# Performance work log

Hardware: AMD Instinct MI355X
Metric: run time of the kernel (lower is better)

Reference implementation:

```python
import jax, jax.numpy as jnp
import numpy as np

B, F, T, EPT, S, E, H, LVL = 16384, 512, 4, 2, 2, 256, 128, 2

def _ple_level(xs_task, x_sh, w_task, b_task, w_sh, b_sh, w_gate, b_gate, w_gsh=None, b_gsh=None):
    # xs_task: [T,B,I] per-task inputs; x_sh: [B,I] shared input
    task_out = jax.nn.relu(jnp.einsum('tbi,teio->tbeo', xs_task, w_task) + b_task[:, None])  # [T,B,EPT,E]
    sh_out = jax.nn.relu(jnp.einsum('bi,sio->bso', x_sh, w_sh) + b_sh)                       # [B,S,E]
    t = task_out.shape[0]
    experts = jnp.concatenate([task_out, jnp.broadcast_to(sh_out[None], (t,) + sh_out.shape)], axis=2)  # [T,B,EPT+S,E]
    gate = jax.nn.softmax(jnp.einsum('tbi,tig->tbg', xs_task, w_gate) + b_gate[:, None], axis=-1)
    task_next = jnp.einsum('tbg,tbge->tbe', gate, experts)  # [T,B,E]
    sh_next = None
    if w_gsh is not None:
        # all experts ordered task0_exp0, task0_exp1, task1_exp0, ..., then shared
        bsz = x_sh.shape[0]
        all_exp = jnp.concatenate([jnp.transpose(task_out, (1, 0, 2, 3)).reshape(bsz, -1, task_out.shape[-1]), sh_out], axis=1)
        gsh = jax.nn.softmax(x_sh @ w_gsh + b_gsh, axis=-1)
        sh_next = jnp.einsum('bg,bge->be', gsh, all_exp)
    return task_next, sh_next

def setup_inputs() -> dict:
    key = jax.random.key(0)
    ks = jax.random.split(key, 16)
    sc = 0.02
    d = {
        'x': jax.random.normal(ks[0], (B, F), jnp.float32),
        # level 0 (in_dim=F, has shared gate)
        'w_task0': jax.random.normal(ks[1], (T, EPT, F, E), jnp.float32) * sc,
        'b_task0': jnp.zeros((T, EPT, E), jnp.float32),
        'w_sh0': jax.random.normal(ks[2], (S, F, E), jnp.float32) * sc,
        'b_sh0': jnp.zeros((S, E), jnp.float32),
        'w_gate0': jax.random.normal(ks[3], (T, F, EPT + S), jnp.float32) * sc,
        'b_gate0': jnp.zeros((T, EPT + S), jnp.float32),
        'w_gsh0': jax.random.normal(ks[4], (F, T * EPT + S), jnp.float32) * sc,
        'b_gsh0': jnp.zeros((T * EPT + S,), jnp.float32),
        # level 1 (last; in_dim=E, no shared gate)
        'w_task1': jax.random.normal(ks[5], (T, EPT, E, E), jnp.float32) * sc,
        'b_task1': jnp.zeros((T, EPT, E), jnp.float32),
        'w_sh1': jax.random.normal(ks[6], (S, E, E), jnp.float32) * sc,
        'b_sh1': jnp.zeros((S, E), jnp.float32),
        'w_gate1': jax.random.normal(ks[7], (T, E, EPT + S), jnp.float32) * sc,
        'b_gate1': jnp.zeros((T, EPT + S), jnp.float32),
        # towers
        'w_tw': jax.random.normal(ks[8], (T, E, H), jnp.float32) * sc,
        'b_tw': jnp.zeros((T, H), jnp.float32),
        'w_out': jax.random.normal(ks[9], (T, H, 2), jnp.float32) * sc,
        'b_out': jnp.zeros((T, 2), jnp.float32),
    }
    return d

def reference(x, w_task0, b_task0, w_sh0, b_sh0, w_gate0, b_gate0, w_gsh0, b_gsh0,
              w_task1, b_task1, w_sh1, b_sh1, w_gate1, b_gate1,
              w_tw, b_tw, w_out, b_out):
    xs_task = jnp.broadcast_to(x[None], (T,) + x.shape)  # all tasks see same input at level 0
    t1, sh1 = _ple_level(xs_task, x, w_task0, b_task0, w_sh0, b_sh0, w_gate0, b_gate0, w_gsh0, b_gsh0)
    t2, _ = _ple_level(t1, sh1, w_task1, b_task1, w_sh1, b_sh1, w_gate1, b_gate1)
    h = jax.nn.relu(jnp.einsum('tbe,teh->tbh', t2, w_tw) + b_tw[:, None])
    logits = jnp.einsum('tbh,tho->tbo', h, w_out) + b_out[:, None]
    p = jax.nn.softmax(logits, axis=-1)
    return jnp.clip(p, 1e-15, 1.0 - 1e-15)  # [T,B,2]
```

## Files before the change

### kernel.cpp

```cpp
#include <hip/hip_runtime.h>

typedef unsigned short u16;
typedef __bf16 bf16x8 __attribute__((ext_vector_type(8)));
typedef float f32x4 __attribute__((ext_vector_type(4)));
typedef u16 u16x8 __attribute__((ext_vector_type(8)));

#define B_ 16384

__device__ __forceinline__ u16 f2b(float f){
  unsigned u = __builtin_bit_cast(unsigned, f);
  u = (u + 0x7FFFu + ((u >> 16) & 1u)) >> 16;
  return (u16)u;
}
__device__ __forceinline__ float b2f(u16 v){
  return __builtin_bit_cast(float, ((unsigned)v) << 16);
}
__device__ __forceinline__ void ld8(const u16* __restrict__ p, float* f){
  u16x8 v = *(const u16x8*)p;
  #pragma unroll
  for (int j = 0; j < 8; ++j) f[j] = b2f(v[j]);
}
__device__ __forceinline__ void st8(u16* __restrict__ p, const float* f){
  u16x8 v;
  #pragma unroll
  for (int j = 0; j < 8; ++j) v[j] = f2b(f[j]);
  *(u16x8*)p = v;
}

__device__ __forceinline__ void gload16(const u16* g, u16* lds){
  __builtin_amdgcn_global_load_lds(
      (const __attribute__((address_space(1))) unsigned int*)g,
      (__attribute__((address_space(3))) unsigned int*)lds, 16, 0, 0);
}

__device__ __forceinline__ void core32(const u16* __restrict__ A,
                                       const u16* __restrict__ Wt,
                                       int K, int m0, int n0, int nt,
                                       u16* sm, f32x4 acc[4][4])
{
  const int tid = threadIdx.x, lane = tid & 63, wave = tid >> 6;
  const int wm = ((tid >> 7) & 3) * 64;
  const int wn = ((tid >> 6) & 1) * 64;

  #pragma unroll
  for (int m = 0; m < 4; ++m)
    #pragma unroll
    for (int n = 0; n < 4; ++n) acc[m][n] = (f32x4){0.f, 0.f, 0.f, 0.f};

  const int s_    = (lane & 7) ^ ((lane >> 3) & 7);
  const int srow2 = 2 * (lane >> 3) + (s_ >> 2);
  const int sk    = (s_ & 3) * 8;
  const u16* gsrc[3];
  int gdst[3];
  #pragma unroll
  for (int i = 0; i < 3; ++i) {
    int c = wave * 3 + i;
    if (c < 16) {
      gsrc[i] = A + (size_t)(m0 + c * 16 + srow2) * K + sk;
      gdst[i] = c * 512;
    } else {
      gsrc[i] = Wt + (size_t)(n0 + (c - 16) * 16 + srow2) * K + sk;
      gdst[i] = 8192 + (c - 16) * 512;
    }
  }

  int aoff[4], boff[4];
  #pragma unroll
  for (int m = 0; m < 4; ++m) {
    int r = wm + m * 16 + (lane & 15);
    int L = r >> 1;
    int phys = (((r & 1) << 2) + (lane >> 4)) ^ (L & 7);
    aoff[m] = L * 64 + phys * 8;
  }
  #pragma unroll
  for (int n = 0; n < 4; ++n) {
    int r = wn + n * 16 + (lane & 15);
    int L = r >> 1;
    int phys = (((r & 1) << 2) + (lane >> 4)) ^ (L & 7);
    boff[n] = 8192 + L * 64 + phys * 8;
  }

  #pragma unroll
  for (int j = 0; j < 2; ++j) {
    u16* sl = sm + j * 12288;
    #pragma unroll
    for (int i = 0; i < 3; ++i) gload16(gsrc[i] + j * 32, sl + gdst[i]);
  }
  asm volatile("s_waitcnt vmcnt(3)" ::: "memory");
  __builtin_amdgcn_s_barrier();

  int cs = 0;
  for (int j = 0; j < nt; ++j) {
    if (j + 2 < nt) {
      int ns = cs + 2; ns = (ns >= 3) ? ns - 3 : ns;
      u16* sl = sm + ns * 12288;
      #pragma unroll
      for (int i = 0; i < 3; ++i) gload16(gsrc[i] + (size_t)(j + 2) * 32, sl + gdst[i]);
    }
    const u16* sa = sm + cs * 12288;
    bf16x8 av[4], bv[4];
    #pragma unroll
    for (int m = 0; m < 4; ++m) av[m] = *(const bf16x8*)(sa + aoff[m]);
    #pragma unroll
    for (int n = 0; n < 4; ++n) bv[n] = *(const bf16x8*)(sa + boff[n]);
    __builtin_amdgcn_s_setprio(1);
    #pragma unroll
    for (int m = 0; m < 4; ++m)
      #pragma unroll
      for (int n = 0; n < 4; ++n)
        acc[m][n] = __builtin_amdgcn_mfma_f32_16x16x32_bf16(av[m], bv[n], acc[m][n], 0, 0, 0);
    __builtin_amdgcn_s_setprio(0);
    if (j + 2 < nt)      asm volatile("s_waitcnt vmcnt(3)" ::: "memory");
    else if (j + 1 < nt) asm volatile("s_waitcnt vmcnt(0)" ::: "memory");
    __builtin_amdgcn_s_barrier();
    cs = (cs == 2) ? 0 : cs + 1;
  }
}


__global__ __launch_bounds__(512) void k_gemm0(const u16* __restrict__ xb,
    const u16* __restrict__ Wt0, const float* __restrict__ bias0,
    u16* __restrict__ E0, float* __restrict__ G0L)
{
  __shared__ __align__(16) u16 sm[36864];
  f32x4 acc[4][4];
  const int bid = blockIdx.x;
  const int swz = (bid & 7) * 168 + (bid >> 3);
  const int m0 = (swz / 21) * 256, n0 = (swz % 21) * 128;
  core32(xb, Wt0, 512, m0, n0, 16, sm, acc);
  const int lane = threadIdx.x & 63;
  const int wm = ((threadIdx.x >> 7) & 3) * 64, wn = ((threadIdx.x >> 6) & 1) * 64;
  #pragma unroll
  for (int mi = 0; mi < 4; ++mi)
    #pragma unroll
    for (int ni = 0; ni < 4; ++ni) {
      int gcol = n0 + wn + ni * 16 + (lane & 15);
      float bias = bias0[gcol];
      #pragma unroll
      for (int q = 0; q < 4; ++q) {
        int grow = m0 + wm + mi * 16 + ((lane >> 4) << 2) + q;
        float v = acc[mi][ni][q] + bias;
        if (gcol < 2560)      E0[(size_t)grow * 2560 + gcol] = f2b(fmaxf(v, 0.f));
        else if (gcol < 2586) G0L[(size_t)grow * 26 + (gcol - 2560)] = v;
      }
    }
}

__global__ __launch_bounds__(256) void k_mix0(const u16* __restrict__ E0,
    const float* __restrict__ G0L, const float* __restrict__ WG1T,
    const float* __restrict__ b_gate1, u16* __restrict__ T1SH,
    float* __restrict__ G1S)
{
  const int b = blockIdx.x * 8 + (threadIdx.x >> 5);
  const int e0 = (threadIdx.x & 31) * 8;
  const float* gl = G0L + (size_t)b * 26;
  float g[4][4];
  #pragma unroll
  for (int t = 0; t < 4; ++t) {
    float l0 = gl[t*4+0], l1 = gl[t*4+1], l2 = gl[t*4+2], l3 = gl[t*4+3];
    float m = fmaxf(fmaxf(l0, l1), fmaxf(l2, l3));
    float e0e = expf(l0-m), e1 = expf(l1-m), e2 = expf(l2-m), e3 = expf(l3-m);
    float inv = 1.f / (e0e + e1 + e2 + e3);
    g[t][0] = e0e*inv; g[t][1] = e1*inv; g[t][2] = e2*inv; g[t][3] = e3*inv;
  }
  float gs[10];
  {
    float m = gl[16];
    #pragma unroll
    for (int j = 1; j < 10; ++j) m = fmaxf(m, gl[16 + j]);
    float s = 0.f;
    #pragma unroll
    for (int j = 0; j < 10; ++j) { gs[j] = expf(gl[16 + j] - m); s += gs[j]; }
    float inv = 1.f / s;
    #pragma unroll
    for (int j = 0; j < 10; ++j) gs[j] *= inv;
  }
  const u16* row = E0 + (size_t)b * 2560;
  float sh0[8], sh1[8], shacc[8];
  ld8(row + 2048 + e0, sh0);
  ld8(row + 2304 + e0, sh1);
  #pragma unroll
  for (int j = 0; j < 8; ++j) shacc[j] = gs[8]*sh0[j] + gs[9]*sh1[j];
  float gp[16];
  #pragma unroll
  for (int t = 0; t < 4; ++t) {
    float te0[8], te1[8], v[8];
    ld8(row + (t*2+0)*256 + e0, te0);
    ld8(row + (t*2+1)*256 + e0, te1);
    #pragma unroll
    for (int j = 0; j < 8; ++j) {
      v[j] = g[t][0]*te0[j] + g[t][1]*te1[j] + g[t][2]*sh0[j] + g[t][3]*sh1[j];
      shacc[j] += gs[t*2+0]*te0[j] + gs[t*2+1]*te1[j];
    }
    st8(T1SH + ((size_t)t * B_ + b) * 256 + e0, v);
    #pragma unroll
    for (int gg = 0; gg < 4; ++gg) {
      const float* wv = WG1T + ((size_t)(t * 4 + gg) * 256 + e0);
      float s = 0.f;
      #pragma unroll
      for (int j = 0; j < 8; ++j) s += v[j] * wv[j];
      gp[t * 4 + gg] = s;
    }
  }
  st8(T1SH + ((size_t)4 * B_ + b) * 256 + e0, shacc);
  #pragma unroll
  for (int i = 0; i < 16; ++i) {
    #pragma unroll
    for (int off = 1; off < 32; off <<= 1)
      gp[i] += __shfl_xor(gp[i], off, 32);
  }
  if ((threadIdx.x & 31) == 0) {
    float* orow = G1S + (size_t)b * 16;
    #pragma unroll
    for (int z = 0; z < 4; ++z) {
      float l0 = gp[z*4+0] + b_gate1[z*4+0];
      float l1 = gp[z*4+1] + b_gate1[z*4+1];
      float l2 = gp[z*4+2] + b_gate1[z*4+2];
      float l3 = gp[z*4+3] + b_gate1[z*4+3];
      float m = fmaxf(fmaxf(l0, l1), fmaxf(l2, l3));
      float x0 = expf(l0-m), x1 = expf(l1-m), x2 = expf(l2-m), x3 = expf(l3-m);
      float inv = 1.f / (x0 + x1 + x2 + x3);
      orow[z*4+0] = x0*inv; orow[z*4+1] = x1*inv;
      orow[z*4+2] = x2*inv; orow[z*4+3] = x3*inv;
    }
  }
}

__global__ __launch_bounds__(512) void k_gemm1(const u16* __restrict__ T1SH,
    const u16* __restrict__ Wt1, const float* __restrict__ bias1,
    u16* __restrict__ E1, u16* __restrict__ SH1E)
{
  __shared__ __align__(16) u16 sm[36864];
  f32x4 acc[4][4];
  const int bid = blockIdx.x;
  const int swz = (bid & 7) * 160 + (bid >> 3);
  const int mi_ = swz / 20, pan = swz % 20;
  const int z  = pan >> 2;
  const int n0 = (pan & 3) * 128;
  const int m0 = mi_ * 256;
  core32(T1SH + (size_t)z * B_ * 256, Wt1 + (size_t)z * 512 * 256, 256, m0, n0, 8, sm, acc);
  const int lane = threadIdx.x & 63;
  const int wm = ((threadIdx.x >> 7) & 3) * 64, wn = ((threadIdx.x >> 6) & 1) * 64;
  const float* bias = bias1 + z * 512;
  #pragma unroll
  for (int mi = 0; mi < 4; ++mi)
    #pragma unroll
    for (int ni = 0; ni < 4; ++ni) {
      int gcol = n0 + wn + ni * 16 + (lane & 15);
      float bv = bias[gcol];
      #pragma unroll
      for (int q = 0; q < 4; ++q) {
        int grow = m0 + wm + mi * 16 + ((lane >> 4) << 2) + q;
        float v = fmaxf(acc[mi][ni][q] + bv, 0.f);
        if (z < 4) E1[((size_t)z * B_ + grow) * 512 + gcol] = f2b(v);
        else       SH1E[(size_t)grow * 512 + gcol] = f2b(v);
      }
    }
}

__global__ __launch_bounds__(256) void k_tower2(const u16* __restrict__ E1,
    const u16* __restrict__ SH1E, const float* __restrict__ G1S,
    const u16* __restrict__ Wtw, const float* __restrict__ b_tw,
    const float* __restrict__ w_out, const float* __restrict__ b_out,
    float* __restrict__ out)
{
  __shared__ __align__(16) u16 sm[32768];
  __shared__ float part[2][128][2];
  f32x4 acc[4][4];
  const int z = blockIdx.z;
  const int m0 = blockIdx.x * 128;
  const int tid = threadIdx.x, lane = tid & 63, wave = tid >> 6;
  const int wm = ((tid >> 7) & 1) * 64, wn = ((tid >> 6) & 1) * 64;

  #pragma unroll
  for (int mi = 0; mi < 4; ++mi)
    #pragma unroll
    for (int ni = 0; ni < 4; ++ni) acc[mi][ni] = (f32x4){0.f, 0.f, 0.f, 0.f};

  const int srow  = lane >> 3;
  const int gslot = (lane & 7) ^ srow;
  const int koff0 = gslot * 8;

  int growA[4], adst[4], bdst[4];
  const u16* bsrc[4];
  #pragma unroll
  for (int i = 0; i < 4; ++i) {
    int c = wave * 4 + i;
    growA[i] = m0 + c * 8 + srow;
    adst[i]  = c * 512;
    bsrc[i]  = Wtw + (size_t)z * 128 * 256 + (size_t)(c * 8 + srow) * 256 + koff0;
    bdst[i]  = 8192 + c * 512;
  }
  const u16* E1z = E1 + (size_t)z * B_ * 512;

  int aoff[2][4], boff[2][4];
  #pragma unroll
  for (int kk = 0; kk < 2; ++kk) {
    #pragma unroll
    for (int m = 0; m < 4; ++m) {
      int r = wm + m * 16 + (lane & 15);
      aoff[kk][m] = r * 64 + (((kk * 4 + (lane >> 4)) ^ (r & 7)) * 8);
    }
    #pragma unroll
    for (int n = 0; n < 4; ++n) {
      int r = wn + n * 16 + (lane & 15);
      boff[kk][n] = 8192 + r * 64 + (((kk * 4 + (lane >> 4)) ^ (r & 7)) * 8);
    }
  }

  #define STAGE_T(J, BUF) do {                                                 \
    u16* buf_ = (BUF);                                                         \
    _Pragma("unroll")                                                          \
    for (int i_ = 0; i_ < 4; ++i_) {                                           \
      size_t eoff_ = (size_t)growA[i_] * 512 + (J) * 64 + koff0;               \
      u16x8 ea_ = *(const u16x8*)(E1z + eoff_);                                \
      u16x8 eb_ = *(const u16x8*)(E1z + eoff_ + 256);                          \
      u16x8 sa_ = *(const u16x8*)(SH1E + eoff_);                               \
      u16x8 sb_ = *(const u16x8*)(SH1E + eoff_ + 256);                         \
      float4 g_ = *(const float4*)(G1S + (size_t)growA[i_] * 16 + z * 4);      \
      u16x8 o_;                                                                \
      _Pragma("unroll")                                                        \
      for (int jj_ = 0; jj_ < 8; ++jj_)                                        \
        o_[jj_] = f2b(g_.x * b2f(ea_[jj_]) + g_.y * b2f(eb_[jj_])              \
                    + g_.z * b2f(sa_[jj_]) + g_.w * b2f(sb_[jj_]));            \
      *(uint4*)(buf_ + adst[i_] + lane * 8) = __builtin_bit_cast(uint4, o_);   \
      gload16(bsrc[i_] + (J) * 64, buf_ + bdst[i_]);                           \
    }                                                                          \
  } while (0)

  STAGE_T(0, sm);
  __syncthreads();

  #pragma unroll
  for (int t = 0; t < 4; ++t) {
    if (t + 1 < 4) STAGE_T(t + 1, sm + ((t + 1) & 1) * 16384);
    const u16* sa = sm + (t & 1) * 16384;
    #pragma unroll
    for (int kk = 0; kk < 2; ++kk) {
      bf16x8 av[4], bv[4];
      #pragma unroll
      for (int m = 0; m < 4; ++m) av[m] = *(const bf16x8*)(sa + aoff[kk][m]);
      #pragma unroll
      for (int n = 0; n < 4; ++n) bv[n] = *(const bf16x8*)(sa + boff[kk][n]);
      #pragma unroll
      for (int m = 0; m < 4; ++m)
        #pragma unroll
        for (int n = 0; n < 4; ++n)
          acc[m][n] = __builtin_amdgcn_mfma_f32_16x16x32_bf16(av[m], bv[n], acc[m][n], 0, 0, 0);
    }
    if (t + 1 < 4) __syncthreads();
  }
  #undef STAGE_T

  #pragma unroll
  for (int mi = 0; mi < 4; ++mi) {
    #pragma unroll
    for (int r = 0; r < 4; ++r) {
      float p0 = 0.f, p1 = 0.f;
      #pragma unroll
      for (int ni = 0; ni < 4; ++ni) {
        int col = wn + ni * 16 + (lane & 15);
        float h = fmaxf(acc[mi][ni][r] + b_tw[z * 128 + col], 0.f);
        p0 += h * w_out[(z * 128 + col) * 2 + 0];
        p1 += h * w_out[(z * 128 + col) * 2 + 1];
      }
      #pragma unroll
      for (int off = 1; off < 16; off <<= 1) {
        p0 += __shfl_xor(p0, off);
        p1 += __shfl_xor(p1, off);
      }
      if ((lane & 15) == 0) {
        int rowl = wm + mi * 16 + ((lane >> 4) << 2) + r;
        part[wn >> 6][rowl][0] = p0;
        part[wn >> 6][rowl][1] = p1;
      }
    }
  }
  __syncthreads();
  if (threadIdx.x < 128) {
    int rowl = threadIdx.x;
    float l0 = part[0][rowl][0] + part[1][rowl][0] + b_out[z * 2 + 0];
    float l1 = part[0][rowl][1] + part[1][rowl][1] + b_out[z * 2 + 1];
    float mx = fmaxf(l0, l1);
    float e0 = expf(l0 - mx), e1 = expf(l1 - mx);
    float inv = 1.f / (e0 + e1);
    float p0 = fminf(fmaxf(e0 * inv, 1e-15f), 1.0f);
    float p1 = fminf(fmaxf(e1 * inv, 1e-15f), 1.0f);
    size_t o = ((size_t)z * B_ + m0 + rowl) * 2;
    out[o] = p0; out[o + 1] = p1;
  }
}

__global__ void k_prep(const float* __restrict__ x,
    const float* __restrict__ w_task0, const float* __restrict__ b_task0,
    const float* __restrict__ w_sh0,   const float* __restrict__ b_sh0,
    const float* __restrict__ w_gate0, const float* __restrict__ b_gate0,
    const float* __restrict__ w_gsh0,  const float* __restrict__ b_gsh0,
    const float* __restrict__ w_task1, const float* __restrict__ b_task1,
    const float* __restrict__ w_sh1,   const float* __restrict__ b_sh1,
    const float* __restrict__ w_gate1, const float* __restrict__ w_tw,
    u16* __restrict__ xb, u16* __restrict__ Wt0, float* __restrict__ bias0,
    u16* __restrict__ Wt1, float* __restrict__ bias1, u16* __restrict__ Wtw,
    float* __restrict__ WG1T)
{
  size_t i = (size_t)blockIdx.x * 256 + threadIdx.x;
  const size_t S_X8  = (size_t)16384 * 512 / 8;
  const size_t S_WT0 = (size_t)2816 * 512;
  const size_t S_B0  = 2816;
  const size_t S_WT1 = (size_t)5 * 512 * 256;
  const size_t S_B1  = 5 * 512;
  const size_t S_WTW = (size_t)4 * 128 * 256;
  const size_t S_WG1 = 4096;

  if (i < S_X8) {
    size_t o = i * 8;
    float4 a = *(const float4*)(x + o);
    float4 b = *(const float4*)(x + o + 4);
    u16x8 v;
    v[0] = f2b(a.x); v[1] = f2b(a.y); v[2] = f2b(a.z); v[3] = f2b(a.w);
    v[4] = f2b(b.x); v[5] = f2b(b.y); v[6] = f2b(b.z); v[7] = f2b(b.w);
    *(u16x8*)(xb + o) = v;
    return;
  }
  i -= S_X8;
  if (i < S_WT0) {
    int c = (int)(i / 512), f = (int)(i % 512);
    float v = 0.f;
    if (c < 2048)      { int te = c >> 8, o = c & 255; v = w_task0[((size_t)te * 512 + f) * 256 + o]; }
    else if (c < 2560) { int s = (c - 2048) >> 8, o = c & 255; v = w_sh0[((size_t)s * 512 + f) * 256 + o]; }
    else if (c < 2576) { int q = c - 2560; int t = q >> 2, gg = q & 3; v = w_gate0[((size_t)t * 512 + f) * 4 + gg]; }
    else if (c < 2586) { int j = c - 2576; v = w_gsh0[(size_t)f * 10 + j]; }
    Wt0[i] = f2b(v);
    return;
  }
  i -= S_WT0;
  if (i < S_B0) {
    int c = (int)i; float v = 0.f;
    if (c < 2048)      { int te = c >> 8, o = c & 255; v = b_task0[te * 256 + o]; }
    else if (c < 2560) { int s = (c - 2048) >> 8, o = c & 255; v = b_sh0[s * 256 + o]; }
    else if (c < 2576) { v = b_gate0[c - 2560]; }
    else if (c < 2586) { v = b_gsh0[c - 2576]; }
    bias0[c] = v;
    return;
  }
  i -= S_B0;
  if (i < S_WT1) {
    int z = (int)(i / (512 * 256)); int rem = (int)(i % (512 * 256));
    int c = rem / 256, f = rem % 256;
    float v;
    if (z < 4) { int ee = c >> 8, o = c & 255; v = w_task1[(((size_t)(z * 2 + ee)) * 256 + f) * 256 + o]; }
    else       { int s = c >> 8, o = c & 255; v = w_sh1[((size_t)s * 256 + f) * 256 + o]; }
    Wt1[i] = f2b(v);
    return;
  }
  i -= S_WT1;
  if (i < S_B1) {
    int z = (int)(i / 512); int c = (int)(i % 512);
    float v;
    if (z < 4) { int ee = c >> 8, o = c & 255; v = b_task1[(z * 2 + ee) * 256 + o]; }
    else       { int s = c >> 8, o = c & 255; v = b_sh1[s * 256 + o]; }
    bias1[(size_t)z * 512 + c] = v;
    return;
  }
  i -= S_B1;
  if (i < S_WTW) {
    int z = (int)(i / (128 * 256)); int rem = (int)(i % (128 * 256));
    int h = rem / 256, f = rem % 256;
    Wtw[i] = f2b(w_tw[((size_t)z * 256 + f) * 128 + h]);
    return;
  }
  i -= S_WTW;
  if (i < S_WG1) {
    int t = (int)(i >> 10), gg = (int)((i >> 8) & 3), e = (int)(i & 255);
    WG1T[i] = w_gate1[((size_t)t * 256 + e) * 4 + gg];
    return;
  }
}

extern "C" void kernel_launch(void* const* d_in, const int* in_sizes, int n_in,
                              void* d_out, int out_size, void* d_ws, size_t ws_size,
                              hipStream_t stream)
{
  (void)in_sizes; (void)n_in; (void)out_size; (void)ws_size;
  const float* x       = (const float*)d_in[0];
  const float* w_task0 = (const float*)d_in[1];
  const float* b_task0 = (const float*)d_in[2];
  const float* w_sh0   = (const float*)d_in[3];
  const float* b_sh0   = (const float*)d_in[4];
  const float* w_gate0 = (const float*)d_in[5];
  const float* b_gate0 = (const float*)d_in[6];
  const float* w_gsh0  = (const float*)d_in[7];
  const float* b_gsh0  = (const float*)d_in[8];
  const float* w_task1 = (const float*)d_in[9];
  const float* b_task1 = (const float*)d_in[10];
  const float* w_sh1   = (const float*)d_in[11];
  const float* b_sh1   = (const float*)d_in[12];
  const float* w_gate1 = (const float*)d_in[13];
  const float* b_gate1 = (const float*)d_in[14];
  const float* w_tw    = (const float*)d_in[15];
  const float* b_tw    = (const float*)d_in[16];
  const float* w_out   = (const float*)d_in[17];
  const float* b_out   = (const float*)d_in[18];
  float* out = (float*)d_out;

  char* ws = (char*)d_ws;
  u16*   XB    = (u16*)  (ws + 0);
  u16*   SH1E  = (u16*)  (ws + 0);
  u16*   WT0   = (u16*)  (ws + 16777216);
  float* BIAS0 = (float*)(ws + 19660800);
  u16*   WT1   = (u16*)  (ws + 19672064);
  float* BIAS1 = (float*)(ws + 20982784);
  u16*   WTW   = (u16*)  (ws + 20993024);
  u16*   E0    = (u16*)  (ws + 21255168);
  float* G0L   = (float*)(ws + 105141248);
  u16*   T1SH  = (u16*)  (ws + 106845184);
  u16*   E1    = (u16*)  (ws + 148788224);
  float* G1S   = (float*)(ws + 215897088);
  float* WG1T  = (float*)(ws + 216945664);

  k_prep<<<12837, 256, 0, stream>>>(x, w_task0, b_task0, w_sh0, b_sh0, w_gate0, b_gate0,
      w_gsh0, b_gsh0, w_task1, b_task1, w_sh1, b_sh1, w_gate1, w_tw,
      XB, WT0, BIAS0, WT1, BIAS1, WTW, WG1T);
  k_gemm0<<<1344, 512, 0, stream>>>(XB, WT0, BIAS0, E0, G0L);
  k_mix0<<<2048, 256, 0, stream>>>(E0, G0L, WG1T, b_gate1, T1SH, G1S);
  k_gemm1<<<1280, 512, 0, stream>>>(T1SH, WT1, BIAS1, E1, SH1E);
  k_tower2<<<dim3(128, 1, 4), 256, 0, stream>>>(E1, SH1E, G1S, WTW, b_tw, w_out, b_out, out);
}
```

Before: 172.0 us.

## Move gate logits out of GEMM0 into mix kernel and retile GEMMs to 128x256

```diff
diff --git a/kernel.cpp b/kernel.cpp
--- a/kernel.cpp
+++ b/kernel.cpp
@@ -33,38 +33,38 @@
       (__attribute__((address_space(3))) unsigned int*)lds, 16, 0, 0);
 }
 
-__device__ __forceinline__ void core32(const u16* __restrict__ A,
-                                       const u16* __restrict__ Wt,
-                                       int K, int m0, int n0, int nt,
-                                       u16* sm, f32x4 acc[4][4])
+__device__ __forceinline__ void core32w(const u16* __restrict__ A,
+                                        const u16* __restrict__ Wt,
+                                        int K, int m0, int n0, int nt,
+                                        u16* sm, f32x4 acc[4][8])
 {
   const int tid = threadIdx.x, lane = tid & 63, wave = tid >> 6;
-  const int wm = ((tid >> 7) & 3) * 64;
-  const int wn = ((tid >> 6) & 1) * 64;
+  const int wm = ((tid >> 7) & 1) * 64;
+  const int wn = ((tid >> 6) & 1) * 128;
 
   #pragma unroll
   for (int m = 0; m < 4; ++m)
     #pragma unroll
-    for (int n = 0; n < 4; ++n) acc[m][n] = (f32x4){0.f, 0.f, 0.f, 0.f};
+    for (int n = 0; n < 8; ++n) acc[m][n] = (f32x4){0.f, 0.f, 0.f, 0.f};
 
   const int s_    = (lane & 7) ^ ((lane >> 3) & 7);
   const int srow2 = 2 * (lane >> 3) + (s_ >> 2);
   const int sk    = (s_ & 3) * 8;
-  const u16* gsrc[3];
-  int gdst[3];
-  #pragma unroll
-  for (int i = 0; i < 3; ++i) {
-    int c = wave * 3 + i;
-    if (c < 16) {
+  const u16* gsrc[6];
+  int gdst[6];
+  #pragma unroll
+  for (int i = 0; i < 6; ++i) {
+    int c = wave * 6 + i;
+    if (c < 8) {
       gsrc[i] = A + (size_t)(m0 + c * 16 + srow2) * K + sk;
       gdst[i] = c * 512;
     } else {
-      gsrc[i] = Wt + (size_t)(n0 + (c - 16) * 16 + srow2) * K + sk;
-      gdst[i] = 8192 + (c - 16) * 512;
-    }
-  }
-
-  int aoff[4], boff[4];
+      gsrc[i] = Wt + (size_t)(n0 + (c - 8) * 16 + srow2) * K + sk;
+      gdst[i] = 4096 + (c - 8) * 512;
+    }
+  }
+
+  int aoff[4], boff[8];
   #pragma unroll
   for (int m = 0; m < 4; ++m) {
     int r = wm + m * 16 + (lane & 15);
@@ -73,20 +73,20 @@
     aoff[m] = L * 64 + phys * 8;
   }
   #pragma unroll
-  for (int n = 0; n < 4; ++n) {
+  for (int n = 0; n < 8; ++n) {
     int r = wn + n * 16 + (lane & 15);
     int L = r >> 1;
     int phys = (((r & 1) << 2) + (lane >> 4)) ^ (L & 7);
-    boff[n] = 8192 + L * 64 + phys * 8;
+    boff[n] = 4096 + L * 64 + phys * 8;
   }
 
   #pragma unroll
   for (int j = 0; j < 2; ++j) {
     u16* sl = sm + j * 12288;
     #pragma unroll
-    for (int i = 0; i < 3; ++i) gload16(gsrc[i] + j * 32, sl + gdst[i]);
-  }
-  asm volatile("s_waitcnt vmcnt(3)" ::: "memory");
+    for (int i = 0; i < 6; ++i) gload16(gsrc[i] + j * 32, sl + gdst[i]);
+  }
+  asm volatile("s_waitcnt vmcnt(6)" ::: "memory");
   __builtin_amdgcn_s_barrier();
 
   int cs = 0;
@@ -95,22 +95,22 @@
       int ns = cs + 2; ns = (ns >= 3) ? ns - 3 : ns;
       u16* sl = sm + ns * 12288;
       #pragma unroll
-      for (int i = 0; i < 3; ++i) gload16(gsrc[i] + (size_t)(j + 2) * 32, sl + gdst[i]);
+      for (int i = 0; i < 6; ++i) gload16(gsrc[i] + (size_t)(j + 2) * 32, sl + gdst[i]);
     }
     const u16* sa = sm + cs * 12288;
-    bf16x8 av[4], bv[4];
+    bf16x8 av[4], bv[8];
     #pragma unroll
     for (int m = 0; m < 4; ++m) av[m] = *(const bf16x8*)(sa + aoff[m]);
     #pragma unroll
-    for (int n = 0; n < 4; ++n) bv[n] = *(const bf16x8*)(sa + boff[n]);
+    for (int n = 0; n < 8; ++n) bv[n] = *(const bf16x8*)(sa + boff[n]);
     __builtin_amdgcn_s_setprio(1);
     #pragma unroll
     for (int m = 0; m < 4; ++m)
       #pragma unroll
-      for (int n = 0; n < 4; ++n)
+      for (int n = 0; n < 8; ++n)
         acc[m][n] = __builtin_amdgcn_mfma_f32_16x16x32_bf16(av[m], bv[n], acc[m][n], 0, 0, 0);
     __builtin_amdgcn_s_setprio(0);
-    if (j + 2 < nt)      asm volatile("s_waitcnt vmcnt(3)" ::: "memory");
+    if (j + 2 < nt)      asm volatile("s_waitcnt vmcnt(6)" ::: "memory");
     else if (j + 1 < nt) asm volatile("s_waitcnt vmcnt(0)" ::: "memory");
     __builtin_amdgcn_s_barrier();
     cs = (cs == 2) ? 0 : cs + 1;
@@ -118,46 +118,62 @@
 }
 
 
-__global__ __launch_bounds__(512) void k_gemm0(const u16* __restrict__ xb,
+__global__ __launch_bounds__(256, 2) void k_gemm0(const u16* __restrict__ xb,
     const u16* __restrict__ Wt0, const float* __restrict__ bias0,
-    u16* __restrict__ E0, float* __restrict__ G0L)
+    u16* __restrict__ E0)
 {
   __shared__ __align__(16) u16 sm[36864];
-  f32x4 acc[4][4];
+  f32x4 acc[4][8];
   const int bid = blockIdx.x;
-  const int swz = (bid & 7) * 168 + (bid >> 3);
-  const int m0 = (swz / 21) * 256, n0 = (swz % 21) * 128;
-  core32(xb, Wt0, 512, m0, n0, 16, sm, acc);
+  const int swz = (bid & 7) * 160 + (bid >> 3);
+  const int m0 = (swz / 10) * 128, n0 = (swz % 10) * 256;
+  core32w(xb, Wt0, 512, m0, n0, 16, sm, acc);
   const int lane = threadIdx.x & 63;
-  const int wm = ((threadIdx.x >> 7) & 3) * 64, wn = ((threadIdx.x >> 6) & 1) * 64;
+  const int wm = ((threadIdx.x >> 7) & 1) * 64, wn = ((threadIdx.x >> 6) & 1) * 128;
   #pragma unroll
   for (int mi = 0; mi < 4; ++mi)
     #pragma unroll
-    for (int ni = 0; ni < 4; ++ni) {
+    for (int ni = 0; ni < 8; ++ni) {
       int gcol = n0 + wn + ni * 16 + (lane & 15);
       float bias = bias0[gcol];
       #pragma unroll
       for (int q = 0; q < 4; ++q) {
         int grow = m0 + wm + mi * 16 + ((lane >> 4) << 2) + q;
-        float v = acc[mi][ni][q] + bias;
-        if (gcol < 2560)      E0[(size_t)grow * 2560 + gcol] = f2b(fmaxf(v, 0.f));
-        else if (gcol < 2586) G0L[(size_t)grow * 26 + (gcol - 2560)] = v;
+        E0[(size_t)grow * 2560 + gcol] = f2b(fmaxf(acc[mi][ni][q] + bias, 0.f));
       }
     }
 }
 
 __global__ __launch_bounds__(256) void k_mix0(const u16* __restrict__ E0,
-    const float* __restrict__ G0L, const float* __restrict__ WG1T,
-    const float* __restrict__ b_gate1, u16* __restrict__ T1SH,
-    float* __restrict__ G1S)
+    const u16* __restrict__ xb, const u16* __restrict__ WG0T,
+    const float* __restrict__ b_gate0, const float* __restrict__ b_gsh0,
+    const float* __restrict__ WG1T, const float* __restrict__ b_gate1,
+    u16* __restrict__ T1SH, float* __restrict__ G1S)
 {
   const int b = blockIdx.x * 8 + (threadIdx.x >> 5);
-  const int e0 = (threadIdx.x & 31) * 8;
-  const float* gl = G0L + (size_t)b * 26;
+  const int l32 = threadIdx.x & 31;
+  const int e0 = l32 * 8;
+
+  float xf[16];
+  ld8(xb + (size_t)b * 512 + l32 * 16, xf);
+  ld8(xb + (size_t)b * 512 + l32 * 16 + 8, xf + 8);
+  float lg[26];
+  #pragma unroll
+  for (int g = 0; g < 26; ++g) {
+    float w0[8], w1[8];
+    ld8(WG0T + (size_t)g * 512 + l32 * 16, w0);
+    ld8(WG0T + (size_t)g * 512 + l32 * 16 + 8, w1);
+    float s = 0.f;
+    #pragma unroll
+    for (int j = 0; j < 8; ++j) s += xf[j] * w0[j] + xf[8 + j] * w1[j];
+    #pragma unroll
+    for (int off = 1; off < 32; off <<= 1) s += __shfl_xor(s, off, 32);
+    lg[g] = s + ((g < 16) ? b_gate0[g] : b_gsh0[g - 16]);
+  }
   float g[4][4];
   #pragma unroll
   for (int t = 0; t < 4; ++t) {
-    float l0 = gl[t*4+0], l1 = gl[t*4+1], l2 = gl[t*4+2], l3 = gl[t*4+3];
+    float l0 = lg[t*4+0], l1 = lg[t*4+1], l2 = lg[t*4+2], l3 = lg[t*4+3];
     float m = fmaxf(fmaxf(l0, l1), fmaxf(l2, l3));
     float e0e = expf(l0-m), e1 = expf(l1-m), e2 = expf(l2-m), e3 = expf(l3-m);
     float inv = 1.f / (e0e + e1 + e2 + e3);
@@ -165,16 +181,17 @@
   }
   float gs[10];
   {
-    float m = gl[16];
-    #pragma unroll
-    for (int j = 1; j < 10; ++j) m = fmaxf(m, gl[16 + j]);
+    float m = lg[16];
+    #pragma unroll
+    for (int j = 1; j < 10; ++j) m = fmaxf(m, lg[16 + j]);
     float s = 0.f;
     #pragma unroll
-    for (int j = 0; j < 10; ++j) { gs[j] = expf(gl[16 + j] - m); s += gs[j]; }
+    for (int j = 0; j < 10; ++j) { gs[j] = expf(lg[16 + j] - m); s += gs[j]; }
     float inv = 1.f / s;
     #pragma unroll
     for (int j = 0; j < 10; ++j) gs[j] *= inv;
   }
+
   const u16* row = E0 + (size_t)b * 2560;
   float sh0[8], sh1[8], shacc[8];
   ld8(row + 2048 + e0, sh0);
@@ -209,7 +226,7 @@
     for (int off = 1; off < 32; off <<= 1)
       gp[i] += __shfl_xor(gp[i], off, 32);
   }
-  if ((threadIdx.x & 31) == 0) {
+  if (l32 == 0) {
     float* orow = G1S + (size_t)b * 16;
     #pragma unroll
     for (int z = 0; z < 4; ++z) {
@@ -226,26 +243,26 @@
   }
 }
 
-__global__ __launch_bounds__(512) void k_gemm1(const u16* __restrict__ T1SH,
+__global__ __launch_bounds__(256, 2) void k_gemm1(const u16* __restrict__ T1SH,
     const u16* __restrict__ Wt1, const float* __restrict__ bias1,
     u16* __restrict__ E1, u16* __restrict__ SH1E)
 {
   __shared__ __align__(16) u16 sm[36864];
-  f32x4 acc[4][4];
+  f32x4 acc[4][8];
   const int bid = blockIdx.x;
   const int swz = (bid & 7) * 160 + (bid >> 3);
-  const int mi_ = swz / 20, pan = swz % 20;
-  const int z  = pan >> 2;
-  const int n0 = (pan & 3) * 128;
-  const int m0 = mi_ * 256;
-  core32(T1SH + (size_t)z * B_ * 256, Wt1 + (size_t)z * 512 * 256, 256, m0, n0, 8, sm, acc);
+  const int mi_ = swz / 10, pan = swz % 10;
+  const int z  = pan >> 1;
+  const int n0 = (pan & 1) * 256;
+  const int m0 = mi_ * 128;
+  core32w(T1SH + (size_t)z * B_ * 256, Wt1 + (size_t)z * 512 * 256, 256, m0, n0, 8, sm, acc);
   const int lane = threadIdx.x & 63;
-  const int wm = ((threadIdx.x >> 7) & 3) * 64, wn = ((threadIdx.x >> 6) & 1) * 64;
+  const int wm = ((threadIdx.x >> 7) & 1) * 64, wn = ((threadIdx.x >> 6) & 1) * 128;
   const float* bias = bias1 + z * 512;
   #pragma unroll
   for (int mi = 0; mi < 4; ++mi)
     #pragma unroll
-    for (int ni = 0; ni < 4; ++ni) {
+    for (int ni = 0; ni < 8; ++ni) {
       int gcol = n0 + wn + ni * 16 + (lane & 15);
       float bv = bias[gcol];
       #pragma unroll
@@ -394,22 +411,22 @@
 __global__ void k_prep(const float* __restrict__ x,
     const float* __restrict__ w_task0, const float* __restrict__ b_task0,
     const float* __restrict__ w_sh0,   const float* __restrict__ b_sh0,
-    const float* __restrict__ w_gate0, const float* __restrict__ b_gate0,
-    const float* __restrict__ w_gsh0,  const float* __restrict__ b_gsh0,
+    const float* __restrict__ w_gate0, const float* __restrict__ w_gsh0,
     const float* __restrict__ w_task1, const float* __restrict__ b_task1,
     const float* __restrict__ w_sh1,   const float* __restrict__ b_sh1,
     const float* __restrict__ w_gate1, const float* __restrict__ w_tw,
     u16* __restrict__ xb, u16* __restrict__ Wt0, float* __restrict__ bias0,
     u16* __restrict__ Wt1, float* __restrict__ bias1, u16* __restrict__ Wtw,
-    float* __restrict__ WG1T)
+    u16* __restrict__ WG0T, float* __restrict__ WG1T)
 {
   size_t i = (size_t)blockIdx.x * 256 + threadIdx.x;
   const size_t S_X8  = (size_t)16384 * 512 / 8;
-  const size_t S_WT0 = (size_t)2816 * 512;
-  const size_t S_B0  = 2816;
+  const size_t S_WT0 = (size_t)2560 * 512;
+  const size_t S_B0  = 2560;
   const size_t S_WT1 = (size_t)5 * 512 * 256;
   const size_t S_B1  = 5 * 512;
   const size_t S_WTW = (size_t)4 * 128 * 256;
+  const size_t S_WG0 = 26 * 512;
   const size_t S_WG1 = 4096;
 
   if (i < S_X8) {
@@ -425,21 +442,17 @@
   i -= S_X8;
   if (i < S_WT0) {
     int c = (int)(i / 512), f = (int)(i % 512);
-    float v = 0.f;
-    if (c < 2048)      { int te = c >> 8, o = c & 255; v = w_task0[((size_t)te * 512 + f) * 256 + o]; }
-    else if (c < 2560) { int s = (c - 2048) >> 8, o = c & 255; v = w_sh0[((size_t)s * 512 + f) * 256 + o]; }
-    else if (c < 2576) { int q = c - 2560; int t = q >> 2, gg = q & 3; v = w_gate0[((size_t)t * 512 + f) * 4 + gg]; }
-    else if (c < 2586) { int j = c - 2576; v = w_gsh0[(size_t)f * 10 + j]; }
+    float v;
+    if (c < 2048) { int te = c >> 8, o = c & 255; v = w_task0[((size_t)te * 512 + f) * 256 + o]; }
+    else          { int s = (c - 2048) >> 8, o = c & 255; v = w_sh0[((size_t)s * 512 + f) * 256 + o]; }
     Wt0[i] = f2b(v);
     return;
   }
   i -= S_WT0;
   if (i < S_B0) {
-    int c = (int)i; float v = 0.f;
-    if (c < 2048)      { int te = c >> 8, o = c & 255; v = b_task0[te * 256 + o]; }
-    else if (c < 2560) { int s = (c - 2048) >> 8, o = c & 255; v = b_sh0[s * 256 + o]; }
-    else if (c < 2576) { v = b_gate0[c - 2560]; }
-    else if (c < 2586) { v = b_gsh0[c - 2576]; }
+    int c = (int)i; float v;
+    if (c < 2048) { int te = c >> 8, o = c & 255; v = b_task0[te * 256 + o]; }
+    else          { int s = (c - 2048) >> 8, o = c & 255; v = b_sh0[s * 256 + o]; }
     bias0[c] = v;
     return;
   }
@@ -470,6 +483,15 @@
     return;
   }
   i -= S_WTW;
+  if (i < S_WG0) {
+    int g = (int)(i / 512), f = (int)(i % 512);
+    float v;
+    if (g < 16) { int t = g >> 2, gg = g & 3; v = w_gate0[((size_t)t * 512 + f) * 4 + gg]; }
+    else        { v = w_gsh0[(size_t)f * 10 + (g - 16)]; }
+    WG0T[i] = f2b(v);
+    return;
+  }
+  i -= S_WG0;
   if (i < S_WG1) {
     int t = (int)(i >> 10), gg = (int)((i >> 8) & 3), e = (int)(i & 255);
     WG1T[i] = w_gate1[((size_t)t * 256 + e) * 4 + gg];
@@ -507,22 +529,22 @@
   u16*   XB    = (u16*)  (ws + 0);
   u16*   SH1E  = (u16*)  (ws + 0);
   u16*   WT0   = (u16*)  (ws + 16777216);
-  float* BIAS0 = (float*)(ws + 19660800);
-  u16*   WT1   = (u16*)  (ws + 19672064);
-  float* BIAS1 = (float*)(ws + 20982784);
-  u16*   WTW   = (u16*)  (ws + 20993024);
-  u16*   E0    = (u16*)  (ws + 21255168);
-  float* G0L   = (float*)(ws + 105141248);
-  u16*   T1SH  = (u16*)  (ws + 106845184);
-  u16*   E1    = (u16*)  (ws + 148788224);
-  float* G1S   = (float*)(ws + 215897088);
-  float* WG1T  = (float*)(ws + 216945664);
-
-  k_prep<<<12837, 256, 0, stream>>>(x, w_task0, b_task0, w_sh0, b_sh0, w_gate0, b_gate0,
-      w_gsh0, b_gsh0, w_task1, b_task1, w_sh1, b_sh1, w_gate1, w_tw,
-      XB, WT0, BIAS0, WT1, BIAS1, WTW, WG1T);
-  k_gemm0<<<1344, 512, 0, stream>>>(XB, WT0, BIAS0, E0, G0L);
-  k_mix0<<<2048, 256, 0, stream>>>(E0, G0L, WG1T, b_gate1, T1SH, G1S);
-  k_gemm1<<<1280, 512, 0, stream>>>(T1SH, WT1, BIAS1, E1, SH1E);
+  float* BIAS0 = (float*)(ws + 19398656);
+  u16*   WT1   = (u16*)  (ws + 19408896);
+  float* BIAS1 = (float*)(ws + 20719616);
+  u16*   WTW   = (u16*)  (ws + 20729856);
+  u16*   WG0T  = (u16*)  (ws + 20992000);
+  float* WG1T  = (float*)(ws + 21018624);
+  u16*   E0    = (u16*)  (ws + 21035008);
+  u16*   T1SH  = (u16*)  (ws + 104921088);
+  u16*   E1    = (u16*)  (ws + 146864128);
+  float* G1S   = (float*)(ws + 213972992);
+
+  k_prep<<<12376, 256, 0, stream>>>(x, w_task0, b_task0, w_sh0, b_sh0,
+      w_gate0, w_gsh0, w_task1, b_task1, w_sh1, b_sh1, w_gate1, w_tw,
+      XB, WT0, BIAS0, WT1, BIAS1, WTW, WG0T, WG1T);
+  k_gemm0<<<1280, 256, 0, stream>>>(XB, WT0, BIAS0, E0);
+  k_mix0<<<2048, 256, 0, stream>>>(E0, XB, WG0T, b_gate0, b_gsh0, WG1T, b_gate1, T1SH, G1S);
+  k_gemm1<<<1280, 256, 0, stream>>>(T1SH, WT1, BIAS1, E1, SH1E);
   k_tower2<<<dim3(128, 1, 4), 256, 0, stream>>>(E1, SH1E, G1S, WTW, b_tw, w_out, b_out, out);
 }
```

Result: slower. 181.1 us (+5.3%).

## Retile gemm0 to 128x256 tiles with two waves and 8x8 MFMA per wave

Applied to the files above, without the earlier changes.

```diff
diff --git a/kernel.cpp b/kernel.cpp
--- a/kernel.cpp
+++ b/kernel.cpp
@@ -31,6 +31,89 @@
   __builtin_amdgcn_global_load_lds(
       (const __attribute__((address_space(1))) unsigned int*)g,
       (__attribute__((address_space(3))) unsigned int*)lds, 16, 0, 0);
+}
+
+__device__ __forceinline__ void core128q(const u16* __restrict__ A,
+                                         const u16* __restrict__ Wt,
+                                         int K, int m0, int n0, int nt,
+                                         u16* sm, f32x4 acc[8][8])
+{
+  const int tid = threadIdx.x, lane = tid & 63, wave = tid >> 6;
+  const int wn = wave * 128;
+
+  #pragma unroll
+  for (int m = 0; m < 8; ++m)
+    #pragma unroll
+    for (int n = 0; n < 8; ++n) acc[m][n] = (f32x4){0.f, 0.f, 0.f, 0.f};
+
+  const int s_    = (lane & 7) ^ ((lane >> 3) & 7);
+  const int srow2 = 2 * (lane >> 3) + (s_ >> 2);
+  const int sk    = (s_ & 3) * 8;
+  const u16* gsrc[12];
+  int gdst[12];
+  #pragma unroll
+  for (int i = 0; i < 12; ++i) {
+    int c = wave * 12 + i;
+    if (c < 8) {
+      gsrc[i] = A + (size_t)(m0 + c * 16 + srow2) * K + sk;
+      gdst[i] = c * 512;
+    } else {
+      gsrc[i] = Wt + (size_t)(n0 + (c - 8) * 16 + srow2) * K + sk;
+      gdst[i] = 4096 + (c - 8) * 512;
+    }
+  }
+
+  int aoff[8], boff[8];
+  #pragma unroll
+  for (int m = 0; m < 8; ++m) {
+    int r = m * 16 + (lane & 15);
+    int L = r >> 1;
+    int phys = (((r & 1) << 2) + (lane >> 4)) ^ (L & 7);
+    aoff[m] = L * 64 + phys * 8;
+  }
+  #pragma unroll
+  for (int n = 0; n < 8; ++n) {
+    int r = wn + n * 16 + (lane & 15);
+    int L = r >> 1;
+    int phys = (((r & 1) << 2) + (lane >> 4)) ^ (L & 7);
+    boff[n] = 4096 + L * 64 + phys * 8;
+  }
+
+  #pragma unroll
+  for (int j = 0; j < 2; ++j) {
+    u16* sl = sm + j * 12288;
+    #pragma unroll
+    for (int i = 0; i < 12; ++i) gload16(gsrc[i] + j * 32, sl + gdst[i]);
+  }
+  asm volatile("s_waitcnt vmcnt(12)" ::: "memory");
+  __builtin_amdgcn_s_barrier();
+
+  int cs = 0;
+  for (int j = 0; j < nt; ++j) {
+    if (j + 2 < nt) {
+      int ns = cs + 2; ns = (ns >= 3) ? ns - 3 : ns;
+      u16* sl = sm + ns * 12288;
+      #pragma unroll
+      for (int i = 0; i < 12; ++i) gload16(gsrc[i] + (size_t)(j + 2) * 32, sl + gdst[i]);
+    }
+    const u16* sa = sm + cs * 12288;
+    bf16x8 av[8], bv[8];
+    #pragma unroll
+    for (int m = 0; m < 8; ++m) av[m] = *(const bf16x8*)(sa + aoff[m]);
+    #pragma unroll
+    for (int n = 0; n < 8; ++n) bv[n] = *(const bf16x8*)(sa + boff[n]);
+    __builtin_amdgcn_s_setprio(1);
+    #pragma unroll
+    for (int m = 0; m < 8; ++m)
+      #pragma unroll
+      for (int n = 0; n < 8; ++n)
+        acc[m][n] = __builtin_amdgcn_mfma_f32_16x16x32_bf16(av[m], bv[n], acc[m][n], 0, 0, 0);
+    __builtin_amdgcn_s_setprio(0);
+    if (j + 2 < nt)      asm volatile("s_waitcnt vmcnt(12)" ::: "memory");
+    else if (j + 1 < nt) asm volatile("s_waitcnt vmcnt(0)" ::: "memory");
+    __builtin_amdgcn_s_barrier();
+    cs = (cs == 2) ? 0 : cs + 1;
+  }
 }
 
 __device__ __forceinline__ void core32(const u16* __restrict__ A,
@@ -118,27 +201,27 @@
 }
 
 
-__global__ __launch_bounds__(512) void k_gemm0(const u16* __restrict__ xb,
+__global__ __launch_bounds__(128, 1) void k_gemm0(const u16* __restrict__ xb,
     const u16* __restrict__ Wt0, const float* __restrict__ bias0,
     u16* __restrict__ E0, float* __restrict__ G0L)
 {
   __shared__ __align__(16) u16 sm[36864];
-  f32x4 acc[4][4];
+  f32x4 acc[8][8];
   const int bid = blockIdx.x;
-  const int swz = (bid & 7) * 168 + (bid >> 3);
-  const int m0 = (swz / 21) * 256, n0 = (swz % 21) * 128;
-  core32(xb, Wt0, 512, m0, n0, 16, sm, acc);
+  const int swz = (bid & 7) * 176 + (bid >> 3);
+  const int m0 = (swz / 11) * 128, n0 = (swz % 11) * 256;
+  core128q(xb, Wt0, 512, m0, n0, 16, sm, acc);
   const int lane = threadIdx.x & 63;
-  const int wm = ((threadIdx.x >> 7) & 3) * 64, wn = ((threadIdx.x >> 6) & 1) * 64;
-  #pragma unroll
-  for (int mi = 0; mi < 4; ++mi)
-    #pragma unroll
-    for (int ni = 0; ni < 4; ++ni) {
+  const int wn = (threadIdx.x >> 6) * 128;
+  #pragma unroll
+  for (int mi = 0; mi < 8; ++mi)
+    #pragma unroll
+    for (int ni = 0; ni < 8; ++ni) {
       int gcol = n0 + wn + ni * 16 + (lane & 15);
       float bias = bias0[gcol];
       #pragma unroll
       for (int q = 0; q < 4; ++q) {
-        int grow = m0 + wm + mi * 16 + ((lane >> 4) << 2) + q;
+        int grow = m0 + mi * 16 + ((lane >> 4) << 2) + q;
         float v = acc[mi][ni][q] + bias;
         if (gcol < 2560)      E0[(size_t)grow * 2560 + gcol] = f2b(fmaxf(v, 0.f));
         else if (gcol < 2586) G0L[(size_t)grow * 26 + (gcol - 2560)] = v;
@@ -521,7 +604,7 @@
   k_prep<<<12837, 256, 0, stream>>>(x, w_task0, b_task0, w_sh0, b_sh0, w_gate0, b_gate0,
       w_gsh0, b_gsh0, w_task1, b_task1, w_sh1, b_sh1, w_gate1, w_tw,
       XB, WT0, BIAS0, WT1, BIAS1, WTW, WG1T);
-  k_gemm0<<<1344, 512, 0, stream>>>(XB, WT0, BIAS0, E0, G0L);
+  k_gemm0<<<1408, 128, 0, stream>>>(XB, WT0, BIAS0, E0, G0L);
   k_mix0<<<2048, 256, 0, stream>>>(E0, G0L, WG1T, b_gate1, T1SH, G1S);
   k_gemm1<<<1280, 512, 0, stream>>>(T1SH, WT1, BIAS1, E1, SH1E);
   k_tower2<<<dim3(128, 1, 4), 256, 0, stream>>>(E1, SH1E, G1S, WTW, b_tw, w_out, b_out, out);
```

Measured after the change: 212.2 us. +23.4%, slower.

## Make k_gemm1 blocks process two M tiles with a continuous prefetch pipeline

Applied to the files above, without the earlier changes.

```diff
diff --git a/kernel.cpp b/kernel.cpp
--- a/kernel.cpp
+++ b/kernel.cpp
@@ -233,29 +233,123 @@
   __shared__ __align__(16) u16 sm[36864];
   f32x4 acc[4][4];
   const int bid = blockIdx.x;
-  const int swz = (bid & 7) * 160 + (bid >> 3);
+  const int swz = (bid & 7) * 80 + (bid >> 3);
   const int mi_ = swz / 20, pan = swz % 20;
   const int z  = pan >> 2;
   const int n0 = (pan & 3) * 128;
   const int m0 = mi_ * 256;
-  core32(T1SH + (size_t)z * B_ * 256, Wt1 + (size_t)z * 512 * 256, 256, m0, n0, 8, sm, acc);
-  const int lane = threadIdx.x & 63;
-  const int wm = ((threadIdx.x >> 7) & 3) * 64, wn = ((threadIdx.x >> 6) & 1) * 64;
+  const u16* A  = T1SH + (size_t)z * B_ * 256;
+  const u16* Wt = Wt1 + (size_t)z * 512 * 256;
+  const int K = 256;
+  const size_t AOFF = (size_t)8192 * 256;
+
+  const int tid = threadIdx.x, lane = tid & 63, wave = tid >> 6;
+  const int wm = ((tid >> 7) & 3) * 64;
+  const int wn = ((tid >> 6) & 1) * 64;
+
+  #pragma unroll
+  for (int m = 0; m < 4; ++m)
+    #pragma unroll
+    for (int n = 0; n < 4; ++n) acc[m][n] = (f32x4){0.f, 0.f, 0.f, 0.f};
+
+  const int s_    = (lane & 7) ^ ((lane >> 3) & 7);
+  const int srow2 = 2 * (lane >> 3) + (s_ >> 2);
+  const int sk    = (s_ & 3) * 8;
+  const u16* gsrc[3];
+  int gdst[3];
+  bool aA[3];
+  #pragma unroll
+  for (int i = 0; i < 3; ++i) {
+    int c = wave * 3 + i;
+    if (c < 16) {
+      aA[i] = true;
+      gsrc[i] = A + (size_t)(m0 + c * 16 + srow2) * K + sk;
+      gdst[i] = c * 512;
+    } else {
+      aA[i] = false;
+      gsrc[i] = Wt + (size_t)(n0 + (c - 16) * 16 + srow2) * K + sk;
+      gdst[i] = 8192 + (c - 16) * 512;
+    }
+  }
+
+  int aoff[4], boff[4];
+  #pragma unroll
+  for (int m = 0; m < 4; ++m) {
+    int r = wm + m * 16 + (lane & 15);
+    int L = r >> 1;
+    int phys = (((r & 1) << 2) + (lane >> 4)) ^ (L & 7);
+    aoff[m] = L * 64 + phys * 8;
+  }
+  #pragma unroll
+  for (int n = 0; n < 4; ++n) {
+    int r = wn + n * 16 + (lane & 15);
+    int L = r >> 1;
+    int phys = (((r & 1) << 2) + (lane >> 4)) ^ (L & 7);
+    boff[n] = 8192 + L * 64 + phys * 8;
+  }
+
+  #pragma unroll
+  for (int j = 0; j < 2; ++j) {
+    u16* sl = sm + j * 12288;
+    #pragma unroll
+    for (int i = 0; i < 3; ++i) gload16(gsrc[i] + j * 32, sl + gdst[i]);
+  }
+  asm volatile("s_waitcnt vmcnt(3)" ::: "memory");
+  __builtin_amdgcn_s_barrier();
+
   const float* bias = bias1 + z * 512;
-  #pragma unroll
-  for (int mi = 0; mi < 4; ++mi)
-    #pragma unroll
-    for (int ni = 0; ni < 4; ++ni) {
-      int gcol = n0 + wn + ni * 16 + (lane & 15);
-      float bv = bias[gcol];
-      #pragma unroll
-      for (int q = 0; q < 4; ++q) {
-        int grow = m0 + wm + mi * 16 + ((lane >> 4) << 2) + q;
-        float v = fmaxf(acc[mi][ni][q] + bv, 0.f);
-        if (z < 4) E1[((size_t)z * B_ + grow) * 512 + gcol] = f2b(v);
-        else       SH1E[(size_t)grow * 512 + gcol] = f2b(v);
+  for (int tt = 0; tt < 2; ++tt) {
+    for (int j = 0; j < 8; ++j) {
+      const int s = tt * 8 + j;
+      const int ss = s + 2;
+      if (ss < 16) {
+        const int jt = ss >> 3, jj = ss & 7;
+        u16* sl = sm + (ss % 3) * 12288;
+        #pragma unroll
+        for (int i = 0; i < 3; ++i) {
+          const u16* src = gsrc[i] + (size_t)jj * 32 + ((aA[i] && jt) ? AOFF : 0);
+          gload16(src, sl + gdst[i]);
+        }
       }
-    }
+      const u16* sa = sm + (s % 3) * 12288;
+      bf16x8 av[4], bv[4];
+      #pragma unroll
+      for (int m = 0; m < 4; ++m) av[m] = *(const bf16x8*)(sa + aoff[m]);
+      #pragma unroll
+      for (int n = 0; n < 4; ++n) bv[n] = *(const bf16x8*)(sa + boff[n]);
+      __builtin_amdgcn_s_setprio(1);
+      #pragma unroll
+      for (int m = 0; m < 4; ++m)
+        #pragma unroll
+        for (int n = 0; n < 4; ++n)
+          acc[m][n] = __builtin_amdgcn_mfma_f32_16x16x32_bf16(av[m], bv[n], acc[m][n], 0, 0, 0);
+      __builtin_amdgcn_s_setprio(0);
+      if (ss < 16)          asm volatile("s_waitcnt vmcnt(3)" ::: "memory");
+      else if (s + 1 < 16)  asm volatile("s_waitcnt vmcnt(0)" ::: "memory");
+      __builtin_amdgcn_s_barrier();
+    }
+    const int mbase = m0 + tt * 8192;
+    #pragma unroll
+    for (int mi = 0; mi < 4; ++mi)
+      #pragma unroll
+      for (int ni = 0; ni < 4; ++ni) {
+        int gcol = n0 + wn + ni * 16 + (lane & 15);
+        float bv2 = bias[gcol];
+        #pragma unroll
+        for (int q = 0; q < 4; ++q) {
+          int grow = mbase + wm + mi * 16 + ((lane >> 4) << 2) + q;
+          float v = fmaxf(acc[mi][ni][q] + bv2, 0.f);
+          if (z < 4) E1[((size_t)z * B_ + grow) * 512 + gcol] = f2b(v);
+          else       SH1E[(size_t)grow * 512 + gcol] = f2b(v);
+        }
+      }
+    if (tt == 0) {
+      #pragma unroll
+      for (int m = 0; m < 4; ++m)
+        #pragma unroll
+        for (int n = 0; n < 4; ++n) acc[m][n] = (f32x4){0.f, 0.f, 0.f, 0.f};
+    }
+  }
 }
 
 __global__ __launch_bounds__(256) void k_tower2(const u16* __restrict__ E1,
@@ -523,6 +617,6 @@
       XB, WT0, BIAS0, WT1, BIAS1, WTW, WG1T);
   k_gemm0<<<1344, 512, 0, stream>>>(XB, WT0, BIAS0, E0, G0L);
   k_mix0<<<2048, 256, 0, stream>>>(E0, G0L, WG1T, b_gate1, T1SH, G1S);
-  k_gemm1<<<1280, 512, 0, stream>>>(T1SH, WT1, BIAS1, E1, SH1E);
+  k_gemm1<<<640, 512, 0, stream>>>(T1SH, WT1, BIAS1, E1, SH1E);
   k_tower2<<<dim3(128, 1, 4), 256, 0, stream>>>(E1, SH1E, G1S, WTW, b_tw, w_out, b_out, out);
 }
```

Measured after the change: 182.4 us. 1.06x slower.
